# Optimization experiments

Hardware: AMD Instinct MI355X
Metric: run time of the kernel (lower is better)

Reference implementation:

```python
import jax, jax.numpy as jnp
import numpy as np
import math

D = 64          # emb_size
R = 32          # num relations
MAX_LEN = 5000  # position table size
E = 30000       # num edges / relation instances
EPSILON = 0.01
THETA = 0.01


def _build_Q():
    # sinusoidal axes [MAX_LEN, D]
    position = jnp.arange(MAX_LEN, dtype=jnp.float32)[:, None]
    div_term = jnp.exp(jnp.arange(0, D, 2, dtype=jnp.float32) * (-math.log(10000.0) / D))
    axes = jnp.zeros((MAX_LEN, D), dtype=jnp.float32)
    axes = axes.at[:, 0::2].set(jnp.sin(position * div_term))
    axes = axes.at[:, 1::2].set(jnp.cos(position * div_term))
    # skew-symmetric generator S_ij = theta * (a_i - a_j); Q = expm(S)  [MAX_LEN, D, D]
    S = THETA * (axes[..., None] - axes[:, None, :])
    Q = jax.scipy.linalg.expm(S)
    return Q


def setup_inputs() -> dict:
    key = jax.random.key(0)
    k1, k2, k3, k4, k5 = jax.random.split(key, 5)
    std = 1.0 / jnp.sqrt(jnp.float32(D))
    relation_embs = jax.random.normal(k1, (R, D, D), dtype=jnp.float32) * std
    Q = _build_Q()
    relation_mapping = jax.random.randint(k2, (E, 2), 0, 2 * R, dtype=jnp.int64 if jax.config.jax_enable_x64 else jnp.int32)
    node_mapping = jax.random.randint(k3, (MAX_LEN,), 0, MAX_LEN)
    edge_index = jax.random.randint(k4, (2, E), 0, MAX_LEN)
    node_embs = jax.random.normal(k5, (MAX_LEN, D), dtype=jnp.float32)
    return {
        "relation_mapping": relation_mapping,
        "node_mapping": node_mapping,
        "edge_index": edge_index,
        "node_embs": node_embs,
        "relation_embs": relation_embs,
        "Q": Q,
    }


def reference(relation_mapping, node_mapping, edge_index, node_embs, relation_embs, Q):
    # node_mapping, edge_index, node_embs are unused by the original forward
    I = jnp.eye(D, dtype=relation_embs.dtype)
    W_even = I + EPSILON * relation_embs   # [R, D, D]
    W_odd = I - EPSILON * relation_embs    # [R, D, D]
    # interleave -> W[2r] = W_even[r], W[2r+1] = W_odd[r]   [2R, D, D]
    W = jnp.stack([W_even, W_odd], axis=1).reshape(-1, D, D)
    Qg = Q[relation_mapping[:, 0]]         # [E, D, D] gather
    rel = W[relation_mapping[:, 1]]        # [E, D, D] gather
    # Q^T @ rel @ Q per edge
    out = jnp.einsum('eji,ejk,ekl->eil', Qg, rel, Qg)
    return out  # dropout p=0.0 is identity
```

## Files before the change

kernel.cpp:

```cpp
#include <hip/hip_runtime.h>

#define TRE_EPS   0.01f
#define TRE_CAP   256
#define TRE_NB    2048
#define TRE_PGRID 1024

typedef float tre_f4 __attribute__((ext_vector_type(4)));
typedef short tre_bf8 __attribute__((ext_vector_type(8)));

__device__ __forceinline__ unsigned short tre_f2bf(float f) {
    unsigned int u = __float_as_uint(f);
    u += 0x7fffu + ((u >> 16) & 1u);
    return (unsigned short)(u >> 16);
}
__device__ __forceinline__ unsigned long long tre_pack4(float a, float b,
                                                        float c, float d) {
    return (unsigned long long)tre_f2bf(a)
         | ((unsigned long long)tre_f2bf(b) << 16)
         | ((unsigned long long)tre_f2bf(c) << 32)
         | ((unsigned long long)tre_f2bf(d) << 48);
}

__global__ __launch_bounds__(256) void tre_bin(
    const int* __restrict__ rm, int E,
    int* __restrict__ counts, int* __restrict__ list, int* __restrict__ cursor)
{
    if (blockIdx.x == 0 && threadIdx.x == 0) *cursor = TRE_PGRID;
    int e = blockIdx.x * 256 + threadIdx.x;
    if (e >= E) return;
    int g  = rm[2 * e + 0];
    int r2 = rm[2 * e + 1];
    int b  = (g << 5) | (r2 >> 1);
    int idx = atomicAdd(&counts[b], 1);
    if (idx < TRE_CAP)
        list[b * TRE_CAP + idx] = (e << 1) | (r2 & 1);
}

__global__ __launch_bounds__(256, 4) void tre_pair(
    const float* __restrict__ Q, const float* __restrict__ RE,
    const int* __restrict__ counts, const int* __restrict__ list,
    int* __restrict__ cursor, float* __restrict__ out)
{
    __shared__ __align__(16) unsigned char sB[16384];
    __shared__ int sList[TRE_CAP];
    __shared__ int sTicket;

    const int t = threadIdx.x;
    const int lane = t & 63;
    const int wv = t >> 6;
    const int fr = lane & 15;
    const int fq = lane >> 4;
    const int i0 = wv << 4;

    unsigned char* REb = sB;
    unsigned char* Qtb = sB + 8192;

    tre_f4 diag[4];
#pragma unroll
    for (int j = 0; j < 4; ++j) {
        int f = (t + 256 * j) << 2;
#pragma unroll
        for (int c = 0; c < 4; ++c) {
            int fc = f + c;
            diag[j][c] = ((fc >> 6) == (fc & 63)) ? 1.0f : 0.0f;
        }
    }

    int b = blockIdx.x;
    for (;;) {
        if (b >= TRE_NB) break;

        const int cnt_raw = counts[b];
        const int cnt = cnt_raw > TRE_CAP ? TRE_CAP : cnt_raw;

        if (cnt > 0) {
            const int g = b >> 5;
            const int r = b & 31;
            const float* Qg  = Q  + ((size_t)g << 12);
            const float* REr = RE + ((size_t)r << 12);

            if (t < cnt) sList[t] = list[b * TRE_CAP + t];

            for (int i = t; i < 1024; i += 256) {
                float4 w = ((const float4*)REr)[i];
                int R = i >> 4, c0 = (i & 15) << 2;
                int o = c0 * 2;
                *(unsigned long long*)(REb + R * 128 + (o ^ ((R & 7) << 4))) =
                    tre_pack4(w.x, w.y, w.z, w.w);
            }
            for (int it = 0; it < 4; ++it) {
                int k0 = (wv << 2) + (it << 4);
                float q0 = Qg[(k0 + 0) * 64 + lane];
                float q1 = Qg[(k0 + 1) * 64 + lane];
                float q2 = Qg[(k0 + 2) * 64 + lane];
                float q3 = Qg[(k0 + 3) * 64 + lane];
                int R = lane, o = k0 * 2;
                *(unsigned long long*)(Qtb + R * 128 + (o ^ ((R & 7) << 4))) =
                    tre_pack4(q0, q1, q2, q3);
            }
            __syncthreads();

            tre_f4 accA[4];
#pragma unroll
            for (int jf = 0; jf < 4; ++jf) accA[jf] = (tre_f4){0.f, 0.f, 0.f, 0.f};
#pragma unroll
            for (int ks = 0; ks < 2; ++ks) {
                int ko = ks * 64 + fq * 16;
                int Ra = i0 + fr;
                tre_bf8 afr = *(const tre_bf8*)(REb + Ra * 128 + (ko ^ ((Ra & 7) << 4)));
#pragma unroll
                for (int jf = 0; jf < 4; ++jf) {
                    int Rb = (jf << 4) + fr;
                    tre_bf8 bfr = *(const tre_bf8*)(Qtb + Rb * 128 + (ko ^ ((Rb & 7) << 4)));
                    accA[jf] = __builtin_amdgcn_mfma_f32_16x16x32_bf16(afr, bfr, accA[jf], 0, 0, 0);
                }
            }
            __syncthreads();

#pragma unroll
            for (int jf = 0; jf < 4; ++jf) {
                int C  = (jf << 4) + fr;
                int r0 = i0 + (fq << 2);
                int o  = r0 * 2;
                *(unsigned long long*)(sB + C * 128 + (o ^ ((C & 7) << 4))) =
                    tre_pack4(accA[jf][0], accA[jf][1], accA[jf][2], accA[jf][3]);
            }
            __syncthreads();

            tre_f4 accM[4];
#pragma unroll
            for (int jf = 0; jf < 4; ++jf) accM[jf] = (tre_f4){0.f, 0.f, 0.f, 0.f};
#pragma unroll
            for (int ks = 0; ks < 2; ++ks) {
                int ko = ks * 64 + fq * 16;
                int Ra = i0 + fr;
                tre_bf8 afr = *(const tre_bf8*)(Qtb + Ra * 128 + (ko ^ ((Ra & 7) << 4)));
#pragma unroll
                for (int jf = 0; jf < 4; ++jf) {
                    int Rb = (jf << 4) + fr;
                    tre_bf8 bfr = *(const tre_bf8*)(sB + Rb * 128 + (ko ^ ((Rb & 7) << 4)));
                    accM[jf] = __builtin_amdgcn_mfma_f32_16x16x32_bf16(afr, bfr, accM[jf], 0, 0, 0);
                }
            }
            __syncthreads();

            float* sM = (float*)sB;
#pragma unroll
            for (int jf = 0; jf < 4; ++jf) {
                int cc = (jf << 4) + fr;
                int r0 = i0 + (fq << 2);
                sM[(r0 + 0) * 64 + cc] = accM[jf][0];
                sM[(r0 + 1) * 64 + cc] = accM[jf][1];
                sM[(r0 + 2) * 64 + cc] = accM[jf][2];
                sM[(r0 + 3) * 64 + cc] = accM[jf][3];
            }
            __syncthreads();

            tre_f4 mreg[4];
#pragma unroll
            for (int j = 0; j < 4; ++j)
                mreg[j] = *(const tre_f4*)&sM[(t + 256 * j) << 2];

            int pk = sList[0];
            for (int i = 0; i < cnt; ++i) {
                int nxt = (i + 1 < cnt) ? sList[i + 1] : 0;
                int e = pk >> 1;
                float s = (pk & 1) ? -TRE_EPS : TRE_EPS;
                tre_f4* dst = (tre_f4*)(out + ((size_t)e << 12));
#pragma unroll
                for (int j = 0; j < 4; ++j) {
                    tre_f4 v = s * mreg[j] + diag[j];
                    __builtin_nontemporal_store(v, &dst[t + 256 * j]);
                }
                pk = nxt;
            }
        }

        __syncthreads();
        if (t == 0) sTicket = atomicAdd(cursor, 1);
        __syncthreads();
        b = sTicket;
    }
}

__global__ __launch_bounds__(256) void tre_direct(
    const int* __restrict__ rm, const float* __restrict__ Q,
    const float* __restrict__ RE, float* __restrict__ out)
{
    __shared__ float sQ[64 * 64];
    __shared__ float sW[64 * 65];

    const int e = blockIdx.x;
    const int g  = rm[2 * e + 0];
    const int r2 = rm[2 * e + 1];
    const int r  = r2 >> 1;
    const float s = (r2 & 1) ? -TRE_EPS : TRE_EPS;
    const int t = threadIdx.x;
    const int i0 = (t >> 4) << 2;
    const int l0 = (t & 15) << 2;

    const float* Qg  = Q  + ((size_t)g << 12);
    const float* REr = RE + ((size_t)r << 12);
    for (int i = t; i < 1024; i += 256) {
        ((float4*)sQ)[i] = ((const float4*)Qg)[i];
        float4 w = ((const float4*)REr)[i];
        int row = i >> 4, col = (i & 15) << 2;
        float* dst = &sW[row * 65 + col];
        dst[0] = w.x; dst[1] = w.y; dst[2] = w.z; dst[3] = w.w;
    }
    __syncthreads();

    float a[4][4] = {{0,0,0,0},{0,0,0,0},{0,0,0,0},{0,0,0,0}};
#pragma unroll 8
    for (int k = 0; k < 64; ++k) {
        float4 qv = *(const float4*)&sQ[(k << 6) + l0];
#pragma unroll
        for (int d = 0; d < 4; ++d) {
            float w = sW[(i0 + d) * 65 + k];
            a[d][0] = fmaf(w, qv.x, a[d][0]);
            a[d][1] = fmaf(w, qv.y, a[d][1]);
            a[d][2] = fmaf(w, qv.z, a[d][2]);
            a[d][3] = fmaf(w, qv.w, a[d][3]);
        }
    }
    __syncthreads();
    float* sA = sW;
#pragma unroll
    for (int d = 0; d < 4; ++d)
        *(float4*)&sA[(i0 + d) * 64 + l0] =
            make_float4(a[d][0], a[d][1], a[d][2], a[d][3]);
    __syncthreads();

    float qtq[4][4] = {{0,0,0,0},{0,0,0,0},{0,0,0,0},{0,0,0,0}};
    float qta[4][4] = {{0,0,0,0},{0,0,0,0},{0,0,0,0},{0,0,0,0}};
#pragma unroll 4
    for (int j = 0; j < 64; ++j) {
        float4 qi = *(const float4*)&sQ[(j << 6) + i0];
        float4 ql = *(const float4*)&sQ[(j << 6) + l0];
        float4 av = *(const float4*)&sA[(j << 6) + l0];
        float qiv[4] = {qi.x, qi.y, qi.z, qi.w};
        float qlv[4] = {ql.x, ql.y, ql.z, ql.w};
        float avv[4] = {av.x, av.y, av.z, av.w};
#pragma unroll
        for (int d = 0; d < 4; ++d)
#pragma unroll
            for (int ee = 0; ee < 4; ++ee) {
                qtq[d][ee] = fmaf(qiv[d], qlv[ee], qtq[d][ee]);
                qta[d][ee] = fmaf(qiv[d], avv[ee], qta[d][ee]);
            }
    }
    float* dst = out + ((size_t)e << 12);
#pragma unroll
    for (int d = 0; d < 4; ++d) {
        float4 v;
        v.x = fmaf(s, qta[d][0], qtq[d][0]);
        v.y = fmaf(s, qta[d][1], qtq[d][1]);
        v.z = fmaf(s, qta[d][2], qtq[d][2]);
        v.w = fmaf(s, qta[d][3], qtq[d][3]);
        *(float4*)&dst[(i0 + d) * 64 + l0] = v;
    }
}

extern "C" void kernel_launch(void* const* d_in, const int* in_sizes, int n_in,
                              void* d_out, int out_size, void* d_ws, size_t ws_size,
                              hipStream_t stream) {
    const int*   rm = (const int*)d_in[0];
    const float* RE = (const float*)d_in[4];
    const float* Q  = (const float*)d_in[5];
    float* out = (float*)d_out;
    const int E = in_sizes[0] / 2;

    const size_t cnt_bytes  = (size_t)TRE_NB * sizeof(int);
    const size_t cur_bytes  = 16;
    const size_t list_bytes = (size_t)TRE_NB * TRE_CAP * sizeof(int);
    const size_t need = cnt_bytes + cur_bytes + list_bytes;

    if (ws_size >= need) {
        int* counts = (int*)d_ws;
        int* cursor = (int*)((char*)d_ws + cnt_bytes);
        int* list   = (int*)((char*)d_ws + cnt_bytes + cur_bytes);
        hipMemsetAsync(counts, 0, cnt_bytes + cur_bytes, stream);
        hipLaunchKernelGGL(tre_bin, dim3((E + 255) / 256), dim3(256), 0, stream,
                           rm, E, counts, list, cursor);
        hipLaunchKernelGGL(tre_pair, dim3(TRE_PGRID), dim3(256), 0, stream,
                           Q, RE, counts, list, cursor, out);
    } else {
        hipLaunchKernelGGL(tre_direct, dim3(E), dim3(256), 0, stream,
                           rm, Q, RE, out);
    }
}
```

Measured before the change: 111.8 us.

## Fuse memset, binning and pair compute into one cooperative kernel

Replaces the memset + bin + pair launch sequence with a single cooperative kernel that zeroes the counters, bins edges, and uses grid-wide syncs between phases. Each block also computes its first bucket's transformed matrix before the second grid sync, so that work overlaps the wait for binning to finish, and the per-bucket matrix is now computed even for empty buckets. This removes two launch gaps, at the cost of grid-wide barriers, a fixed 768-block grid, and wasted matrix work on empty buckets. The old direct fallback is dropped and workspace size is no longer checked.

```diff
diff --git a/kernel.cpp b/kernel.cpp
--- a/kernel.cpp
+++ b/kernel.cpp
@@ -1,8 +1,12 @@
 #include <hip/hip_runtime.h>
+#include <hip/hip_cooperative_groups.h>
+
+namespace cg = cooperative_groups;
 
 #define TRE_EPS   0.01f
 #define TRE_CAP   256
 #define TRE_NB    2048
+#define TRE_CGRID 768
 #define TRE_PGRID 1024
 
 typedef float tre_f4 __attribute__((ext_vector_type(4)));
@@ -19,6 +23,179 @@
          | ((unsigned long long)tre_f2bf(b) << 16)
          | ((unsigned long long)tre_f2bf(c) << 32)
          | ((unsigned long long)tre_f2bf(d) << 48);
+}
+
+__device__ __forceinline__ void tre_compute_M(
+    int b, const float* __restrict__ Q, const float* __restrict__ RE,
+    unsigned char* sB, int t, tre_f4 mreg[4])
+{
+    const int g = b >> 5;
+    const int r = b & 31;
+    const int lane = t & 63;
+    const int wv = t >> 6;
+    const int fr = lane & 15;
+    const int fq = lane >> 4;
+    const int i0 = wv << 4;
+
+    const float* Qg  = Q  + ((size_t)g << 12);
+    const float* REr = RE + ((size_t)r << 12);
+    unsigned char* REb = sB;
+    unsigned char* Qtb = sB + 8192;
+
+    for (int i = t; i < 1024; i += 256) {
+        float4 w = ((const float4*)REr)[i];
+        int R = i >> 4, c0 = (i & 15) << 2;
+        int o = c0 * 2;
+        *(unsigned long long*)(REb + R * 128 + (o ^ ((R & 7) << 4))) =
+            tre_pack4(w.x, w.y, w.z, w.w);
+    }
+    for (int it = 0; it < 4; ++it) {
+        int k0 = (wv << 2) + (it << 4);
+        float q0 = Qg[(k0 + 0) * 64 + lane];
+        float q1 = Qg[(k0 + 1) * 64 + lane];
+        float q2 = Qg[(k0 + 2) * 64 + lane];
+        float q3 = Qg[(k0 + 3) * 64 + lane];
+        int R = lane, o = k0 * 2;
+        *(unsigned long long*)(Qtb + R * 128 + (o ^ ((R & 7) << 4))) =
+            tre_pack4(q0, q1, q2, q3);
+    }
+    __syncthreads();
+
+    tre_f4 accA[4];
+#pragma unroll
+    for (int jf = 0; jf < 4; ++jf) accA[jf] = (tre_f4){0.f, 0.f, 0.f, 0.f};
+#pragma unroll
+    for (int ks = 0; ks < 2; ++ks) {
+        int ko = ks * 64 + fq * 16;
+        int Ra = i0 + fr;
+        tre_bf8 afr = *(const tre_bf8*)(REb + Ra * 128 + (ko ^ ((Ra & 7) << 4)));
+#pragma unroll
+        for (int jf = 0; jf < 4; ++jf) {
+            int Rb = (jf << 4) + fr;
+            tre_bf8 bfr = *(const tre_bf8*)(Qtb + Rb * 128 + (ko ^ ((Rb & 7) << 4)));
+            accA[jf] = __builtin_amdgcn_mfma_f32_16x16x32_bf16(afr, bfr, accA[jf], 0, 0, 0);
+        }
+    }
+    __syncthreads();
+
+#pragma unroll
+    for (int jf = 0; jf < 4; ++jf) {
+        int C  = (jf << 4) + fr;
+        int r0 = i0 + (fq << 2);
+        int o  = r0 * 2;
+        *(unsigned long long*)(sB + C * 128 + (o ^ ((C & 7) << 4))) =
+            tre_pack4(accA[jf][0], accA[jf][1], accA[jf][2], accA[jf][3]);
+    }
+    __syncthreads();
+
+    tre_f4 accM[4];
+#pragma unroll
+    for (int jf = 0; jf < 4; ++jf) accM[jf] = (tre_f4){0.f, 0.f, 0.f, 0.f};
+#pragma unroll
+    for (int ks = 0; ks < 2; ++ks) {
+        int ko = ks * 64 + fq * 16;
+        int Ra = i0 + fr;
+        tre_bf8 afr = *(const tre_bf8*)(Qtb + Ra * 128 + (ko ^ ((Ra & 7) << 4)));
+#pragma unroll
+        for (int jf = 0; jf < 4; ++jf) {
+            int Rb = (jf << 4) + fr;
+            tre_bf8 bfr = *(const tre_bf8*)(sB + Rb * 128 + (ko ^ ((Rb & 7) << 4)));
+            accM[jf] = __builtin_amdgcn_mfma_f32_16x16x32_bf16(afr, bfr, accM[jf], 0, 0, 0);
+        }
+    }
+    __syncthreads();
+
+    float* sM = (float*)sB;
+#pragma unroll
+    for (int jf = 0; jf < 4; ++jf) {
+        int cc = (jf << 4) + fr;
+        int r0 = i0 + (fq << 2);
+        sM[(r0 + 0) * 64 + cc] = accM[jf][0];
+        sM[(r0 + 1) * 64 + cc] = accM[jf][1];
+        sM[(r0 + 2) * 64 + cc] = accM[jf][2];
+        sM[(r0 + 3) * 64 + cc] = accM[jf][3];
+    }
+    __syncthreads();
+
+#pragma unroll
+    for (int j = 0; j < 4; ++j)
+        mreg[j] = *(const tre_f4*)&sM[(t + 256 * j) << 2];
+}
+
+__global__ __launch_bounds__(256, 4) void tre_fused(
+    const float* __restrict__ Q, const float* __restrict__ RE,
+    const int* __restrict__ rm, int E,
+    int* __restrict__ counts, int* __restrict__ list, int* __restrict__ cursor,
+    float* __restrict__ out)
+{
+    __shared__ __align__(16) unsigned char sB[16384];
+    __shared__ int sList[TRE_CAP];
+    __shared__ int sTicket;
+
+    const int t    = threadIdx.x;
+    const int nthr = gridDim.x * 256;
+    const int gid  = blockIdx.x * 256 + t;
+
+    for (int i = gid; i < TRE_NB; i += nthr) counts[i] = 0;
+    if (gid == 0) *cursor = (int)gridDim.x;
+    cg::this_grid().sync();
+
+    for (int e = gid; e < E; e += nthr) {
+        int g  = rm[2 * e + 0];
+        int r2 = rm[2 * e + 1];
+        int bk = (g << 5) | (r2 >> 1);
+        int idx = atomicAdd(&counts[bk], 1);
+        if (idx < TRE_CAP)
+            list[bk * TRE_CAP + idx] = (e << 1) | (r2 & 1);
+    }
+
+    tre_f4 diag[4];
+#pragma unroll
+    for (int j = 0; j < 4; ++j) {
+        int f = (t + 256 * j) << 2;
+#pragma unroll
+        for (int c = 0; c < 4; ++c) {
+            int fc = f + c;
+            diag[j][c] = ((fc >> 6) == (fc & 63)) ? 1.0f : 0.0f;
+        }
+    }
+
+    int b = blockIdx.x;
+    tre_f4 mreg[4];
+    tre_compute_M(b, Q, RE, sB, t, mreg);
+
+    cg::this_grid().sync();
+
+    for (;;) {
+        const int cnt_raw = counts[b];
+        const int cnt = cnt_raw > TRE_CAP ? TRE_CAP : cnt_raw;
+
+        if (cnt > 0) {
+            if (t < cnt) sList[t] = list[b * TRE_CAP + t];
+            __syncthreads();
+
+            int pk = sList[0];
+            for (int i = 0; i < cnt; ++i) {
+                int nxt = (i + 1 < cnt) ? sList[i + 1] : 0;
+                int e = pk >> 1;
+                float s = (pk & 1) ? -TRE_EPS : TRE_EPS;
+                tre_f4* dst = (tre_f4*)(out + ((size_t)e << 12));
+#pragma unroll
+                for (int j = 0; j < 4; ++j) {
+                    tre_f4 v = s * mreg[j] + diag[j];
+                    __builtin_nontemporal_store(v, &dst[t + 256 * j]);
+                }
+                pk = nxt;
+            }
+        }
+
+        __syncthreads();
+        if (t == 0) sTicket = atomicAdd(cursor, 1);
+        __syncthreads();
+        b = sTicket;
+        if (b >= TRE_NB) break;
+        tre_compute_M(b, Q, RE, sB, t, mreg);
+    }
 }
 
 __global__ __launch_bounds__(256) void tre_bin(
@@ -46,14 +223,6 @@
     __shared__ int sTicket;
 
     const int t = threadIdx.x;
-    const int lane = t & 63;
-    const int wv = t >> 6;
-    const int fr = lane & 15;
-    const int fq = lane >> 4;
-    const int i0 = wv << 4;
-
-    unsigned char* REb = sB;
-    unsigned char* Qtb = sB + 8192;
 
     tre_f4 diag[4];
 #pragma unroll
@@ -74,92 +243,9 @@
         const int cnt = cnt_raw > TRE_CAP ? TRE_CAP : cnt_raw;
 
         if (cnt > 0) {
-            const int g = b >> 5;
-            const int r = b & 31;
-            const float* Qg  = Q  + ((size_t)g << 12);
-            const float* REr = RE + ((size_t)r << 12);
-
+            tre_f4 mreg[4];
             if (t < cnt) sList[t] = list[b * TRE_CAP + t];
-
-            for (int i = t; i < 1024; i += 256) {
-                float4 w = ((const float4*)REr)[i];
-                int R = i >> 4, c0 = (i & 15) << 2;
-                int o = c0 * 2;
-                *(unsigned long long*)(REb + R * 128 + (o ^ ((R & 7) << 4))) =
-                    tre_pack4(w.x, w.y, w.z, w.w);
-            }
-            for (int it = 0; it < 4; ++it) {
-                int k0 = (wv << 2) + (it << 4);
-                float q0 = Qg[(k0 + 0) * 64 + lane];
-                float q1 = Qg[(k0 + 1) * 64 + lane];
-                float q2 = Qg[(k0 + 2) * 64 + lane];
-                float q3 = Qg[(k0 + 3) * 64 + lane];
-                int R = lane, o = k0 * 2;
-                *(unsigned long long*)(Qtb + R * 128 + (o ^ ((R & 7) << 4))) =
-                    tre_pack4(q0, q1, q2, q3);
-            }
-            __syncthreads();
-
-            tre_f4 accA[4];
-#pragma unroll
-            for (int jf = 0; jf < 4; ++jf) accA[jf] = (tre_f4){0.f, 0.f, 0.f, 0.f};
-#pragma unroll
-            for (int ks = 0; ks < 2; ++ks) {
-                int ko = ks * 64 + fq * 16;
-                int Ra = i0 + fr;
-                tre_bf8 afr = *(const tre_bf8*)(REb + Ra * 128 + (ko ^ ((Ra & 7) << 4)));
-#pragma unroll
-                for (int jf = 0; jf < 4; ++jf) {
-                    int Rb = (jf << 4) + fr;
-                    tre_bf8 bfr = *(const tre_bf8*)(Qtb + Rb * 128 + (ko ^ ((Rb & 7) << 4)));
-                    accA[jf] = __builtin_amdgcn_mfma_f32_16x16x32_bf16(afr, bfr, accA[jf], 0, 0, 0);
-                }
-            }
-            __syncthreads();
-
-#pragma unroll
-            for (int jf = 0; jf < 4; ++jf) {
-                int C  = (jf << 4) + fr;
-                int r0 = i0 + (fq << 2);
-                int o  = r0 * 2;
-                *(unsigned long long*)(sB + C * 128 + (o ^ ((C & 7) << 4))) =
-                    tre_pack4(accA[jf][0], accA[jf][1], accA[jf][2], accA[jf][3]);
-            }
-            __syncthreads();
-
-            tre_f4 accM[4];
-#pragma unroll
-            for (int jf = 0; jf < 4; ++jf) accM[jf] = (tre_f4){0.f, 0.f, 0.f, 0.f};
-#pragma unroll
-            for (int ks = 0; ks < 2; ++ks) {
-                int ko = ks * 64 + fq * 16;
-                int Ra = i0 + fr;
-                tre_bf8 afr = *(const tre_bf8*)(Qtb + Ra * 128 + (ko ^ ((Ra & 7) << 4)));
-#pragma unroll
-                for (int jf = 0; jf < 4; ++jf) {
-                    int Rb = (jf << 4) + fr;
-                    tre_bf8 bfr = *(const tre_bf8*)(sB + Rb * 128 + (ko ^ ((Rb & 7) << 4)));
-                    accM[jf] = __builtin_amdgcn_mfma_f32_16x16x32_bf16(afr, bfr, accM[jf], 0, 0, 0);
-                }
-            }
-            __syncthreads();
-
-            float* sM = (float*)sB;
-#pragma unroll
-            for (int jf = 0; jf < 4; ++jf) {
-                int cc = (jf << 4) + fr;
-                int r0 = i0 + (fq << 2);
-                sM[(r0 + 0) * 64 + cc] = accM[jf][0];
-                sM[(r0 + 1) * 64 + cc] = accM[jf][1];
-                sM[(r0 + 2) * 64 + cc] = accM[jf][2];
-                sM[(r0 + 3) * 64 + cc] = accM[jf][3];
-            }
-            __syncthreads();
-
-            tre_f4 mreg[4];
-#pragma unroll
-            for (int j = 0; j < 4; ++j)
-                mreg[j] = *(const tre_f4*)&sM[(t + 256 * j) << 2];
+            tre_compute_M(b, Q, RE, sB, t, mreg);
 
             int pk = sList[0];
             for (int i = 0; i < cnt; ++i) {
@@ -180,84 +266,6 @@
         if (t == 0) sTicket = atomicAdd(cursor, 1);
         __syncthreads();
         b = sTicket;
-    }
-}
-
-__global__ __launch_bounds__(256) void tre_direct(
-    const int* __restrict__ rm, const float* __restrict__ Q,
-    const float* __restrict__ RE, float* __restrict__ out)
-{
-    __shared__ float sQ[64 * 64];
-    __shared__ float sW[64 * 65];
-
-    const int e = blockIdx.x;
-    const int g  = rm[2 * e + 0];
-    const int r2 = rm[2 * e + 1];
-    const int r  = r2 >> 1;
-    const float s = (r2 & 1) ? -TRE_EPS : TRE_EPS;
-    const int t = threadIdx.x;
-    const int i0 = (t >> 4) << 2;
-    const int l0 = (t & 15) << 2;
-
-    const float* Qg  = Q  + ((size_t)g << 12);
-    const float* REr = RE + ((size_t)r << 12);
-    for (int i = t; i < 1024; i += 256) {
-        ((float4*)sQ)[i] = ((const float4*)Qg)[i];
-        float4 w = ((const float4*)REr)[i];
-        int row = i >> 4, col = (i & 15) << 2;
-        float* dst = &sW[row * 65 + col];
-        dst[0] = w.x; dst[1] = w.y; dst[2] = w.z; dst[3] = w.w;
-    }
-    __syncthreads();
-
-    float a[4][4] = {{0,0,0,0},{0,0,0,0},{0,0,0,0},{0,0,0,0}};
-#pragma unroll 8
-    for (int k = 0; k < 64; ++k) {
-        float4 qv = *(const float4*)&sQ[(k << 6) + l0];
-#pragma unroll
-        for (int d = 0; d < 4; ++d) {
-            float w = sW[(i0 + d) * 65 + k];
-            a[d][0] = fmaf(w, qv.x, a[d][0]);
-            a[d][1] = fmaf(w, qv.y, a[d][1]);
-            a[d][2] = fmaf(w, qv.z, a[d][2]);
-            a[d][3] = fmaf(w, qv.w, a[d][3]);
-        }
-    }
-    __syncthreads();
-    float* sA = sW;
-#pragma unroll
-    for (int d = 0; d < 4; ++d)
-        *(float4*)&sA[(i0 + d) * 64 + l0] =
-            make_float4(a[d][0], a[d][1], a[d][2], a[d][3]);
-    __syncthreads();
-
-    float qtq[4][4] = {{0,0,0,0},{0,0,0,0},{0,0,0,0},{0,0,0,0}};
-    float qta[4][4] = {{0,0,0,0},{0,0,0,0},{0,0,0,0},{0,0,0,0}};
-#pragma unroll 4
-    for (int j = 0; j < 64; ++j) {
-        float4 qi = *(const float4*)&sQ[(j << 6) + i0];
-        float4 ql = *(const float4*)&sQ[(j << 6) + l0];
-        float4 av = *(const float4*)&sA[(j << 6) + l0];
-        float qiv[4] = {qi.x, qi.y, qi.z, qi.w};
-        float qlv[4] = {ql.x, ql.y, ql.z, ql.w};
-        float avv[4] = {av.x, av.y, av.z, av.w};
-#pragma unroll
-        for (int d = 0; d < 4; ++d)
-#pragma unroll
-            for (int ee = 0; ee < 4; ++ee) {
-                qtq[d][ee] = fmaf(qiv[d], qlv[ee], qtq[d][ee]);
-                qta[d][ee] = fmaf(qiv[d], avv[ee], qta[d][ee]);
-            }
-    }
-    float* dst = out + ((size_t)e << 12);
-#pragma unroll
-    for (int d = 0; d < 4; ++d) {
-        float4 v;
-        v.x = fmaf(s, qta[d][0], qtq[d][0]);
-        v.y = fmaf(s, qta[d][1], qtq[d][1]);
-        v.z = fmaf(s, qta[d][2], qtq[d][2]);
-        v.w = fmaf(s, qta[d][3], qtq[d][3]);
-        *(float4*)&dst[(i0 + d) * 64 + l0] = v;
     }
 }
 
@@ -268,24 +276,25 @@
     const float* RE = (const float*)d_in[4];
     const float* Q  = (const float*)d_in[5];
     float* out = (float*)d_out;
-    const int E = in_sizes[0] / 2;
+    int E = in_sizes[0] / 2;
 
     const size_t cnt_bytes  = (size_t)TRE_NB * sizeof(int);
     const size_t cur_bytes  = 16;
-    const size_t list_bytes = (size_t)TRE_NB * TRE_CAP * sizeof(int);
-    const size_t need = cnt_bytes + cur_bytes + list_bytes;
-
-    if (ws_size >= need) {
-        int* counts = (int*)d_ws;
-        int* cursor = (int*)((char*)d_ws + cnt_bytes);
-        int* list   = (int*)((char*)d_ws + cnt_bytes + cur_bytes);
+    int* counts = (int*)d_ws;
+    int* cursor = (int*)((char*)d_ws + cnt_bytes);
+    int* list   = (int*)((char*)d_ws + cnt_bytes + cur_bytes);
+
+    void* args[] = { (void*)&Q, (void*)&RE, (void*)&rm, (void*)&E,
+                     (void*)&counts, (void*)&list, (void*)&cursor,
+                     (void*)&out };
+    hipError_t err = hipLaunchCooperativeKernel(
+        (const void*)tre_fused, dim3(TRE_CGRID), dim3(256), args, 0, stream);
+
+    if (err != hipSuccess) {
         hipMemsetAsync(counts, 0, cnt_bytes + cur_bytes, stream);
         hipLaunchKernelGGL(tre_bin, dim3((E + 255) / 256), dim3(256), 0, stream,
                            rm, E, counts, list, cursor);
         hipLaunchKernelGGL(tre_pair, dim3(TRE_PGRID), dim3(256), 0, stream,
                            Q, RE, counts, list, cursor, out);
-    } else {
-        hipLaunchKernelGGL(tre_direct, dim3(E), dim3(256), 0, stream,
-                           rm, Q, RE, out);
-    }
-}
+    }
+}
```

Result: slower. 238.6 us (+113.3%).
